# Optimization experiments

Hardware: AMD Instinct MI355X
Metric: run time of the kernel (lower is better)

## Reference

```python
import jax, jax.numpy as jnp
import numpy as np

B, H, N, D = 2, 16, 2048, 64

def setup_inputs() -> dict:
    key = jax.random.key(0)
    ks = jax.random.split(key, 5)
    q = jax.random.normal(ks[0], (B, H, N, D), dtype=jnp.float32)
    k = jax.random.normal(ks[1], (B, H, N, D), dtype=jnp.float32)
    v = jax.random.normal(ks[2], (B, H, N, D), dtype=jnp.float32)
    # 1x1 Conv2d(heads, heads, bias=False) == HxH linear mixing over the head dim
    W_pre = jax.random.normal(ks[3], (H, H), dtype=jnp.float32) * (1.0 / jnp.sqrt(H))
    W_post = jax.random.normal(ks[4], (H, H), dtype=jnp.float32) * (1.0 / jnp.sqrt(H))
    return {"q": q, "k": k, "v": v, "W_pre": W_pre, "W_post": W_post}

def reference(q, k, v, W_pre, W_post):
    heads = q.shape[1]
    d_head = q.shape[-1]
    # original: scale = (1/sqrt(heads)) / sqrt(d_head)
    scale = 1.0 / (jnp.sqrt(jnp.float32(heads)) * jnp.sqrt(jnp.float32(d_head)))
    # pre-softmax talking heads applied to BOTH q and k (head-mixing linear)
    q = jnp.einsum('ef,bfnd->bend', W_pre, q)
    k = jnp.einsum('ef,bfnd->bend', W_pre, k)
    attn_weights = jnp.einsum('bhid,bhjd->bhij', q, k) * scale  # [B,H,N,N]
    i = q.shape[-2]
    j = k.shape[-2]
    causal_mask = jnp.triu(jnp.ones((i, j), dtype=bool), k=1)
    attn_weights = jnp.where(causal_mask, -jnp.inf, attn_weights)
    # softmax computed in float32 (dtype=torch.float32 in attn_fn)
    attn_probs = jax.nn.softmax(attn_weights.astype(jnp.float32), axis=-1)
    # dropout p=0.0 -> identity
    attn_probs = jnp.einsum('ef,bfij->beij', W_post, attn_probs)
    attn_output = jnp.einsum('bhij,bhjd->bhid', attn_probs, v)
    return attn_output
```

## Files before the change

kernel.cpp:

```cpp
#include <hip/hip_runtime.h>
#include <math.h>

typedef _Float16 Hh;
typedef __attribute__((ext_vector_type(8))) _Float16 half8;
typedef __attribute__((ext_vector_type(4))) _Float16 half4;
typedef __attribute__((ext_vector_type(4))) float float4v;

#define B_ 2
#define H_ 16
#define N_ 2048
#define D_ 64
#define ND_ (N_*D_)
#define C1 0.04508422f

#define BAR() asm volatile("s_waitcnt lgkmcnt(0)\n\ts_barrier" ::: "memory")

#define EB_JS 324
#define EB_IS 20
#define PM_ES 580
#define PM_IS 36

__global__ __launch_bounds__(256) void prep_kernel(const float* __restrict__ q,
    const float* __restrict__ k, const float* __restrict__ v,
    const float* __restrict__ Wpre,
    Hh* __restrict__ qb, Hh* __restrict__ kb, Hh* __restrict__ vt2,
    float4* __restrict__ out4, float4* __restrict__ lacc4)
{
    int tid = threadIdx.x;
    int bid = blockIdx.x;
    if (bid < 512) {
        __shared__ float wsh[256];
        wsh[tid] = Wpre[tid];
        __syncthreads();
        int tensor = bid >> 8;
        int g = ((bid & 255) << 8) | tid;
        int b = g >> 15;
        int r = g & 32767;
        const float4* src = (const float4*)(tensor ? k : q);
        Hh* dst = tensor ? kb : qb;
        float4 x[16];
        #pragma unroll
        for (int f=0; f<16; f++) x[f] = src[(size_t)(b*16+f)*32768 + r];
        #pragma unroll
        for (int e=0; e<16; e++) {
            float4 a = make_float4(0.f,0.f,0.f,0.f);
            #pragma unroll
            for (int f=0; f<16; f++) {
                float wv = wsh[e*16+f];
                a.x += wv*x[f].x; a.y += wv*x[f].y; a.z += wv*x[f].z; a.w += wv*x[f].w;
            }
            half4 hv; hv[0]=(Hh)a.x; hv[1]=(Hh)a.y; hv[2]=(Hh)a.z; hv[3]=(Hh)a.w;
            *(half4*)(dst + (size_t)(b*16+e)*ND_ + (size_t)r*4) = hv;
        }
    } else if (bid < 768) {
        __shared__ Hh tile[64*48];
        int tb = bid - 512;
        int be = tb >> 3;
        int jtg = tb & 7;
        const float4* v4 = (const float4*)v;
        for (int u=0; u<8; u++) {
            int jt = jtg*8 + u;
            #pragma unroll
            for (int p=0; p<2; p++) {
                int j = p*16 + (tid>>4);
                int d4 = tid & 15;
                float4 val = v4[(size_t)be*32768 + (size_t)(jt*32+j)*16 + d4];
                tile[(d4*4+0)*48 + j] = (Hh)val.x;
                tile[(d4*4+1)*48 + j] = (Hh)val.y;
                tile[(d4*4+2)*48 + j] = (Hh)val.z;
                tile[(d4*4+3)*48 + j] = (Hh)val.w;
            }
            BAR();
            {
                int d = tid >> 2;
                int jc = (tid & 3) * 8;
                half8 o;
                #pragma unroll
                for (int z=0; z<8; z++) o[z] = tile[d*48 + jc + z];
                *(half8*)(vt2 + ((size_t)(be*64) + jt)*2048 + (size_t)tid*8) = o;
            }
            BAR();
        }
    } else {
        int zid = (bid - 768) * 256 + tid;
        float4 zz = make_float4(0.f,0.f,0.f,0.f);
        #pragma unroll
        for (int u=0; u<4; u++) out4[(size_t)u*262144 + zid] = zz;
        if (zid < 16384) lacc4[zid] = zz;
    }
}

__global__ __launch_bounds__(512) void denom_kernel(const Hh* __restrict__ qb,
    const Hh* __restrict__ kb, float* __restrict__ lacc_g)
{
    int bid = blockIdx.x;
    int s = bid & 7;
    int idx = 127 - (bid >> 3);
    int b = idx & 1, it = idx >> 1;
    if (s > it) return;

    int i0 = it * 32;
    int tid = threadIdx.x;
    int lane = tid & 63, w = tid >> 6;
    int qd = lane >> 4, c = lane & 15;
    int f0 = 2*w;

    half8 aq[2][2][2];
    #pragma unroll
    for (int fi=0; fi<2; fi++) {
        #pragma unroll
        for (int ig=0; ig<2; ig++) {
            const Hh* qr = qb + (size_t)((b*16+f0+fi)*N_ + i0 + ig*16 + c)*64 + qd*8;
            aq[fi][ig][0] = *(const half8*)qr;
            aq[fi][ig][1] = *(const half8*)(qr+32);
        }
    }
    float lacc[2][2][4];
    #pragma unroll
    for (int fi=0;fi<2;fi++) for (int ig=0;ig<2;ig++) for (int r=0;r<4;r++) lacc[fi][ig][r]=0.f;

    for (int jt = s; jt <= it; jt += 8) {
        int j0 = jt*32;
        #pragma unroll
        for (int fi=0; fi<2; fi++) {
            #pragma unroll
            for (int jh=0; jh<2; jh++) {
                const Hh* kr = kb + (size_t)((b*16+f0+fi)*N_ + j0 + jh*16 + c)*64 + qd*8;
                half8 b0 = *(const half8*)kr;
                half8 b1 = *(const half8*)(kr+32);
                #pragma unroll
                for (int ig=0; ig<2; ig++) {
                    float4v sv = {0.f,0.f,0.f,0.f};
                    sv = __builtin_amdgcn_mfma_f32_16x16x32_f16(aq[fi][ig][0], b0, sv, 0,0,0);
                    sv = __builtin_amdgcn_mfma_f32_16x16x32_f16(aq[fi][ig][1], b1, sv, 0,0,0);
                    #pragma unroll
                    for (int r=0; r<4; r++) {
                        int i = i0 + ig*16 + qd*4 + r;
                        int j = j0 + jh*16 + c;
                        float ev = (j <= i) ? __builtin_amdgcn_exp2f(sv[r]*C1) : 0.f;
                        lacc[fi][ig][r] += ev;
                    }
                }
            }
        }
    }
    #pragma unroll
    for (int fi=0; fi<2; fi++) {
        #pragma unroll
        for (int ig=0; ig<2; ig++) {
            #pragma unroll
            for (int r=0; r<4; r++) {
                float vs = lacc[fi][ig][r];
                vs += __shfl_xor(vs, 1);
                vs += __shfl_xor(vs, 2);
                vs += __shfl_xor(vs, 4);
                vs += __shfl_xor(vs, 8);
                if (c == 0)
                    unsafeAtomicAdd(&lacc_g[(size_t)(b*16+f0+fi)*N_ + i0 + ig*16 + qd*4 + r], vs);
            }
        }
    }
}

__global__ __launch_bounds__(512,4) void attend_kernel(const Hh* __restrict__ qb,
    const Hh* __restrict__ kb, const Hh* __restrict__ vt2,
    const float* __restrict__ lacc_g, const float* __restrict__ Wpost,
    float* __restrict__ out)
{
    __shared__ Hh Ebuf[32*EB_JS];
    __shared__ Hh Pm[16*PM_ES];

    int bid = blockIdx.x;
    int s = (bid & 7) >> 1;
    int idxp = ((bid >> 3) << 1) | (bid & 1);
    int idx = 255 - idxp;
    int b = idx & 1, it = idx >> 1;
    int jtmax = it >> 1;
    if (s > jtmax) return;
    int i0 = it * 16;

    int tid = threadIdx.x;
    int lane = tid & 63, w = tid >> 6;
    int qd = lane >> 4, c = lane & 15;

    int fg = w & 3, jh = w >> 2;
    half8 aq[4][2];
    float lgr[4][4];
    #pragma unroll
    for (int ff=0; ff<4; ff++) {
        int f = 4*fg + ff;
        const Hh* qr = qb + (size_t)((b*16+f)*N_ + i0 + c)*64 + qd*8;
        aq[ff][0] = *(const half8*)qr;
        aq[ff][1] = *(const half8*)(qr+32);
        #pragma unroll
        for (int r=0; r<4; r++)
            lgr[ff][r] = __builtin_amdgcn_logf(
                lacc_g[(size_t)(b*16+f)*N_ + i0 + qd*4 + r]);
    }
    int jh2 = w & 1, ib = 4*(w>>1);
    half4 wf;
    #pragma unroll
    for (int z=0; z<4; z++) wf[z] = (Hh)Wpost[c*16 + qd*4 + z];

    float4v acc[2][4];
    #pragma unroll
    for (int el=0; el<2; el++) for (int nc=0; nc<4; nc++)
        acc[el][nc] = (float4v){0.f,0.f,0.f,0.f};

    auto scores = [&](int jt) {
        int jc = jt*32 + jh*16;
        float4v sv[4];
        #pragma unroll
        for (int ff=0; ff<4; ff++) {
            int f = 4*fg + ff;
            const Hh* kr = kb + (size_t)((b*16+f)*N_ + jc + c)*64 + qd*8;
            half8 b0 = *(const half8*)kr;
            half8 b1 = *(const half8*)(kr+32);
            float4v t = {0.f,0.f,0.f,0.f};
            t = __builtin_amdgcn_mfma_f32_16x16x32_f16(aq[ff][0], b0, t, 0,0,0);
            t = __builtin_amdgcn_mfma_f32_16x16x32_f16(aq[ff][1], b1, t, 0,0,0);
            sv[ff] = t;
        }
        int j = jc + c;
        #pragma unroll
        for (int r=0; r<4; r++) {
            int i = i0 + qd*4 + r;
            half4 h;
            #pragma unroll
            for (int ff=0; ff<4; ff++)
                h[ff] = (Hh)((j <= i) ? __builtin_amdgcn_exp2f(sv[ff][r]*C1 - lgr[ff][r]) : 0.f);
            *(half4*)&Ebuf[(jh*16+c)*EB_JS + (qd*4+r)*EB_IS + fg*4] = h;
        }
    };

    scores(s);
    BAR();

    for (int jt = s; jt <= jtmax; jt += 4) {
        #pragma unroll
        for (int ii=0; ii<4; ii++) {
            int i = ib + ii;
            half4 ef = *(const half4*)&Ebuf[(jh2*16+c)*EB_JS + i*EB_IS + qd*4];
            float4v cc = {0.f,0.f,0.f,0.f};
            cc = __builtin_amdgcn_mfma_f32_16x16x16f16(ef, wf, cc, 0,0,0);
            half4 hv;
            #pragma unroll
            for (int r=0; r<4; r++) hv[r] = (Hh)cc[r];
            *(half4*)&Pm[c*PM_ES + i*PM_IS + jh2*16 + qd*4] = hv;
        }
        BAR();
        #pragma unroll
        for (int el=0; el<2; el++) {
            int e = 2*w + el;
            half8 pa = *(const half8*)&Pm[e*PM_ES + c*PM_IS + qd*8];
            #pragma unroll
            for (int nc=0; nc<4; nc++) {
                const Hh* vr = vt2 + (size_t)((b*16+e)*64 + jt)*2048 + (nc*16+c)*32 + qd*8;
                half8 vb = *(const half8*)vr;
                acc[el][nc] = __builtin_amdgcn_mfma_f32_16x16x32_f16(pa, vb, acc[el][nc], 0,0,0);
            }
        }
        if (jt + 4 <= jtmax) scores(jt + 4);
        BAR();
    }

    #pragma unroll
    for (int el=0; el<2; el++) {
        int e = 2*w + el;
        #pragma unroll
        for (int nc0=0; nc0<4; nc0++) {
            int nc = (nc0 + s) & 3;
            #pragma unroll
            for (int r=0; r<4; r++)
                unsafeAtomicAdd(&out[(size_t)((b*16+e)*N_ + i0 + qd*4 + r)*64 + nc*16 + c],
                                acc[el][nc][r]);
        }
    }
}

extern "C" void kernel_launch(void* const* d_in, const int* in_sizes, int n_in,
                              void* d_out, int out_size, void* d_ws, size_t ws_size,
                              hipStream_t stream) {
    const float* q     = (const float*)d_in[0];
    const float* k     = (const float*)d_in[1];
    const float* v     = (const float*)d_in[2];
    const float* Wpre  = (const float*)d_in[3];
    const float* Wpost = (const float*)d_in[4];
    float* out = (float*)d_out;

    size_t tsz = (size_t)B_*H_*N_*D_;
    Hh* qb = (Hh*)d_ws;
    Hh* kb = qb + tsz;
    Hh* vt2 = kb + tsz;
    float* lacc = (float*)(vt2 + tsz);

    prep_kernel<<<1792, 256, 0, stream>>>(q, k, v, Wpre, qb, kb, vt2,
                                          (float4*)out, (float4*)lacc);
    denom_kernel<<<1024, 512, 0, stream>>>(qb, kb, lacc);
    attend_kernel<<<1024, 512, 0, stream>>>(qb, kb, vt2, lacc, Wpost, out);
}
```

Measured before the change: 266.4 us.

## Rebalance causal denominator kernel by pairing row tiles and using 1024-thread blocks

```diff
diff --git a/kernel.cpp b/kernel.cpp
--- a/kernel.cpp
+++ b/kernel.cpp
@@ -90,73 +90,72 @@
     }
 }
 
-__global__ __launch_bounds__(512) void denom_kernel(const Hh* __restrict__ qb,
+__global__ __launch_bounds__(1024,4) void denom_kernel(const Hh* __restrict__ qb,
     const Hh* __restrict__ kb, float* __restrict__ lacc_g)
 {
     int bid = blockIdx.x;
     int s = bid & 7;
-    int idx = 127 - (bid >> 3);
-    int b = idx & 1, it = idx >> 1;
-    if (s > it) return;
-
-    int i0 = it * 32;
+    int idx = bid >> 3;
+    int b = idx & 1;
+    int pr = idx >> 1;
     int tid = threadIdx.x;
     int lane = tid & 63, w = tid >> 6;
     int qd = lane >> 4, c = lane & 15;
-    int f0 = 2*w;
-
-    half8 aq[2][2][2];
-    #pragma unroll
-    for (int fi=0; fi<2; fi++) {
-        #pragma unroll
-        for (int ig=0; ig<2; ig++) {
-            const Hh* qr = qb + (size_t)((b*16+f0+fi)*N_ + i0 + ig*16 + c)*64 + qd*8;
-            aq[fi][ig][0] = *(const half8*)qr;
-            aq[fi][ig][1] = *(const half8*)(qr+32);
-        }
-    }
-    float lacc[2][2][4];
-    #pragma unroll
-    for (int fi=0;fi<2;fi++) for (int ig=0;ig<2;ig++) for (int r=0;r<4;r++) lacc[fi][ig][r]=0.f;
-
-    for (int jt = s; jt <= it; jt += 8) {
-        int j0 = jt*32;
-        #pragma unroll
-        for (int fi=0; fi<2; fi++) {
+
+    const Hh* qh = qb + (size_t)(b*16 + w)*ND_;
+    const Hh* kh = kb + (size_t)(b*16 + w)*ND_;
+
+    for (int half = 0; half < 2; half++) {
+        int it = half ? (31 - pr) : pr;
+        int i0 = it * 64;
+
+        half8 aq[4][2];
+        #pragma unroll
+        for (int ig=0; ig<4; ig++) {
+            const Hh* qr = qh + (size_t)(i0 + ig*16 + c)*64 + qd*8;
+            aq[ig][0] = *(const half8*)qr;
+            aq[ig][1] = *(const half8*)(qr+32);
+        }
+        float lacc[4][4];
+        #pragma unroll
+        for (int ig=0; ig<4; ig++)
+            #pragma unroll
+            for (int r=0; r<4; r++) lacc[ig][r] = 0.f;
+
+        int jtmax = 2*it + 1;
+        for (int jt = s; jt <= jtmax; jt += 8) {
+            int j0 = jt*32;
             #pragma unroll
             for (int jh=0; jh<2; jh++) {
-                const Hh* kr = kb + (size_t)((b*16+f0+fi)*N_ + j0 + jh*16 + c)*64 + qd*8;
+                const Hh* kr = kh + (size_t)(j0 + jh*16 + c)*64 + qd*8;
                 half8 b0 = *(const half8*)kr;
                 half8 b1 = *(const half8*)(kr+32);
+                int j = j0 + jh*16 + c;
                 #pragma unroll
-                for (int ig=0; ig<2; ig++) {
+                for (int ig=0; ig<4; ig++) {
                     float4v sv = {0.f,0.f,0.f,0.f};
-                    sv = __builtin_amdgcn_mfma_f32_16x16x32_f16(aq[fi][ig][0], b0, sv, 0,0,0);
-                    sv = __builtin_amdgcn_mfma_f32_16x16x32_f16(aq[fi][ig][1], b1, sv, 0,0,0);
+                    sv = __builtin_amdgcn_mfma_f32_16x16x32_f16(aq[ig][0], b0, sv, 0,0,0);
+                    sv = __builtin_amdgcn_mfma_f32_16x16x32_f16(aq[ig][1], b1, sv, 0,0,0);
                     #pragma unroll
                     for (int r=0; r<4; r++) {
                         int i = i0 + ig*16 + qd*4 + r;
-                        int j = j0 + jh*16 + c;
                         float ev = (j <= i) ? __builtin_amdgcn_exp2f(sv[r]*C1) : 0.f;
-                        lacc[fi][ig][r] += ev;
+                        lacc[ig][r] += ev;
                     }
                 }
             }
         }
-    }
-    #pragma unroll
-    for (int fi=0; fi<2; fi++) {
-        #pragma unroll
-        for (int ig=0; ig<2; ig++) {
+        #pragma unroll
+        for (int ig=0; ig<4; ig++) {
             #pragma unroll
             for (int r=0; r<4; r++) {
-                float vs = lacc[fi][ig][r];
+                float vs = lacc[ig][r];
                 vs += __shfl_xor(vs, 1);
                 vs += __shfl_xor(vs, 2);
                 vs += __shfl_xor(vs, 4);
                 vs += __shfl_xor(vs, 8);
                 if (c == 0)
-                    unsafeAtomicAdd(&lacc_g[(size_t)(b*16+f0+fi)*N_ + i0 + ig*16 + qd*4 + r], vs);
+                    unsafeAtomicAdd(&lacc_g[(size_t)(b*16+w)*N_ + i0 + ig*16 + qd*4 + r], vs);
             }
         }
     }
@@ -296,6 +295,6 @@
 
     prep_kernel<<<1792, 256, 0, stream>>>(q, k, v, Wpre, qb, kb, vt2,
                                           (float4*)out, (float4*)lacc);
-    denom_kernel<<<1024, 512, 0, stream>>>(qb, kb, lacc);
+    denom_kernel<<<256, 1024, 0, stream>>>(qb, kb, lacc);
     attend_kernel<<<1024, 512, 0, stream>>>(qb, kb, vt2, lacc, Wpost, out);
 }
```

Result: faster. 249.0 us (-6.5%).
